# Kernel optimization log

Hardware: AMD Instinct MI355X
Metric: run time of the kernel (lower is better)

The kernel has to match this reference:

```python
import jax, jax.numpy as jnp
import numpy as np

Q = 0.96  # fixed draw from min(1, Uniform(0.9, 1.02)) for determinism


def _tf_quantile(t, q):
    # flatten all but batch dim, linear-interp quantile along last axis
    b = t.shape[0]
    flat = t.reshape(b, -1)
    srt = jnp.sort(flat, axis=-1)
    rank = float(flat.shape[-1])
    pos = (rank - 1.0) * q
    lo = int(np.floor(pos))
    hi = int(np.ceil(pos))
    w_hi = jnp.asarray(pos - lo, dtype=t.dtype)
    return (1.0 - w_hi) * srt[:, lo] + w_hi * srt[:, hi]  # (B,)


def reference(x, v, uu, mask):
    # x: (B, C, L), v: (B, 4, L), uu: (B, Cu, L, L), mask: (B, 1, L) bool
    B, C, L = x.shape
    maskb = mask.astype(bool)
    mask_sum = jnp.sum(maskb.astype(x.dtype), axis=-1)  # (B, 1)
    maxlen = _tf_quantile(mask_sum, Q)                  # (B,) valid count per sample

    # random permutation via argsort: valid slots filled with -1, invalid with U(0,1)
    key = jax.random.key(42)
    rand = jax.random.uniform(key, maskb.shape, dtype=x.dtype)
    rand = jnp.where(~maskb, rand, jnp.asarray(-1.0, x.dtype))
    perm = jnp.argsort(-rand, axis=-1)                  # descending, (B, 1, L)

    mask_p = jnp.take_along_axis(maskb, perm, axis=-1)
    x_p = jnp.take_along_axis(x, jnp.broadcast_to(perm, x.shape), axis=-1)
    v_p = jnp.take_along_axis(v, jnp.broadcast_to(perm, v.shape), axis=-1)
    # permute both particle axes of pairwise features uu: uu[b,c,perm[i],perm[j]]
    uu_p = jnp.take_along_axis(uu, jnp.broadcast_to(perm[:, :, :, None], uu.shape), axis=-2)
    uu_p = jnp.take_along_axis(uu_p, jnp.broadcast_to(perm[:, :, None, :], uu.shape), axis=-1)

    maxlen = jnp.maximum(jnp.round(maxlen), 1.0)        # (B,)
    ml = maxlen.astype(jnp.int32)[:, None, None]        # (B, 1, 1)
    ch = jnp.arange(L, dtype=jnp.int32)[None, None, :]  # (1, 1, L)
    keep = ch < ml                                       # identity when maxlen >= L (tf.cond)
    mask_p = jnp.where(keep, mask_p, jnp.zeros_like(mask_p))
    x_p = jnp.where(keep, x_p, jnp.zeros_like(x_p))
    v_p = jnp.where(keep, v_p, jnp.zeros_like(v_p))
    return (x_p, v_p, mask_p, uu_p)


def setup_inputs() -> dict:
    key = jax.random.key(0)
    k1, k2, k3, k4 = jax.random.split(key, 4)
    B, C, L, Cu = 64, 64, 512, 4
    x = jax.random.normal(k1, (B, C, L), dtype=jnp.float32)
    v = jax.random.normal(k2, (B, 4, L), dtype=jnp.float32)
    uu = jax.random.normal(k3, (B, Cu, L, L), dtype=jnp.float32)
    # realistic ragged mask: first `length` particles valid per sample
    lengths = jax.random.randint(k4, (B, 1, 1), L // 2, L + 1)
    mask = (jnp.arange(L)[None, None, :] < lengths)
    return {"x": x, "v": v, "uu": uu, "mask": mask}
```

## Files before the change

kernel.cpp:

```cpp
#include <hip/hip_runtime.h>
#include <stdint.h>

#define LEN 512
#define NB 64
#define NCX 64
#define NCV 4
#define NCU 4

typedef float f4 __attribute__((ext_vector_type(4)));

__device__ __forceinline__ uint32_t rotl32(uint32_t v, int r) {
  return (v << r) | (v >> (32 - r));
}

__device__ __forceinline__ void threefry2x32_k042(uint32_t c0, uint32_t c1,
                                                  uint32_t& o0, uint32_t& o1) {
  const uint32_t ks0 = 0u, ks1 = 42u;
  const uint32_t ks2 = 0u ^ 42u ^ 0x1BD11BDAu;
  uint32_t x0 = c0 + ks0;
  uint32_t x1 = c1 + ks1;
#define TF_ROUND(R) { x0 += x1; x1 = rotl32(x1, R); x1 ^= x0; }
  TF_ROUND(13) TF_ROUND(15) TF_ROUND(26) TF_ROUND(6)
  x0 += ks1; x1 += ks2 + 1u;
  TF_ROUND(17) TF_ROUND(29) TF_ROUND(16) TF_ROUND(24)
  x0 += ks2; x1 += ks0 + 2u;
  TF_ROUND(13) TF_ROUND(15) TF_ROUND(26) TF_ROUND(6)
  x0 += ks0; x1 += ks1 + 3u;
  TF_ROUND(17) TF_ROUND(29) TF_ROUND(16) TF_ROUND(24)
  x0 += ks1; x1 += ks2 + 4u;
  TF_ROUND(13) TF_ROUND(15) TF_ROUND(26) TF_ROUND(6)
  x0 += ks2; x1 += ks0 + 5u;
#undef TF_ROUND
  o0 = x0; o1 = x1;
}

__global__ __launch_bounds__(LEN) void build_perm(const void* __restrict__ mask,
                                                  int* __restrict__ src,
                                                  int* __restrict__ dst,
                                                  int* __restrict__ ml_arr,
                                                  float* __restrict__ mask_out) {
  const int b = blockIdx.x;
  const int l = threadIdx.x;
  const int wave = l >> 6, lane = l & 63;
  __shared__ alignas(16) uint32_t s_pack[LEN];
  __shared__ int wsum[8];
  __shared__ int woff[9];

  const uint32_t w0 = ((const uint32_t*)mask)[0];
  bool valid;
  if (w0 == 1u) {
    valid = ((const int*)mask)[b * LEN + l] != 0;
  } else if (w0 == 0x3F800000u) {
    valid = ((const float*)mask)[b * LEN + l] != 0.0f;
  } else {
    valid = ((const unsigned char*)mask)[b * LEN + l] != 0;
  }
  const bool inv = !valid;

  uint32_t o0, o1;
  threefry2x32_k042(0u, (uint32_t)(b * LEN + l), o0, o1);
  const uint32_t bits = o0 ^ o1;
  const uint32_t ui = (bits >> 9) | 0x3F800000u;
  const uint32_t me = ((ui & 0x7FFFFFu) << 9) | (uint32_t)(511 - l);

  const unsigned long long bal = __ballot(inv);
  const int lower = __popcll(bal & ((1ull << lane) - 1ull));
  if (lane == 0) wsum[wave] = __popcll(bal);
  __syncthreads();
  if (l == 0) {
    int acc = 0;
    for (int w = 0; w < 8; ++w) { woff[w] = acc; acc += wsum[w]; }
    woff[8] = acc;
  }
  __syncthreads();
  const int n_inv = woff[8];
  const int inv_before = woff[wave] + lower;
  if (inv) {
    s_pack[inv_before] = me;
  }
  __syncthreads();

  int pos;
  if (inv) {
    int rank = 0;
    int j = 0;
    for (; j + 8 <= n_inv; j += 8) {
      const uint4 p0 = *(const uint4*)&s_pack[j];
      const uint4 p1 = *(const uint4*)&s_pack[j + 4];
      rank += (int)(p0.x > me) + (int)(p0.y > me) + (int)(p0.z > me) +
              (int)(p0.w > me) + (int)(p1.x > me) + (int)(p1.y > me) +
              (int)(p1.z > me) + (int)(p1.w > me);
    }
    for (; j < n_inv; ++j) rank += (int)(s_pack[j] > me);
    pos = rank;
  } else {
    pos = n_inv + (l - inv_before);
  }
  src[b * LEN + pos] = l;
  dst[b * LEN + l] = pos;

  const int nv = LEN - n_inv;
  const int ml = nv < 1 ? 1 : nv;
  if (l == 0) ml_arr[b] = ml;
  mask_out[b * LEN + l] = (l >= n_inv && l < ml) ? 1.0f : 0.0f;
}

__global__ __launch_bounds__(256) void uu_perm(const float* __restrict__ in,
                                               float* __restrict__ out,
                                               const float* __restrict__ xin,
                                               const float* __restrict__ vin,
                                               float* __restrict__ xout,
                                               float* __restrict__ vout,
                                               const int* __restrict__ src,
                                               const int* __restrict__ ml_arr) {
  __shared__ float s_row[4][LEN];
  const int tid = threadIdx.x;
  const int wave = tid >> 6, lane = tid & 63;
  const int b = blockIdx.x >> 6;
  const int k = blockIdx.x & 63;
  const int orow0 = blockIdx.x * 32 + wave * 8;
  const int i0 = orow0 & (LEN - 1);
  const long plane = (long)(orow0 & ~(LEN - 1)) * LEN;
  const int* srcb_full = src + b * LEN;

  int rs[8];
#pragma unroll
  for (int r = 0; r < 8; ++r) rs[r] = srcb_full[i0 + r];

  f4 a0[8], a1[8];
#pragma unroll
  for (int r = 0; r < 8; ++r) {
    const float* ip = in + plane + (long)rs[r] * LEN + lane * 4;
    a0[r] = *(const f4*)(ip);
    a1[r] = *(const f4*)(ip + 256);
  }

  int c0[4], c1[4];
#pragma unroll
  for (int kk = 0; kk < 4; ++kk) {
    c0[kk] = srcb_full[lane * 4 + kk];
    c1[kk] = srcb_full[256 + lane * 4 + kk];
  }

  float* myrow = &s_row[wave][0];
  float* op0 = out + plane + (long)i0 * LEN + lane * 4;

#pragma unroll
  for (int r = 0; r < 8; ++r) {
    *(f4*)(myrow + lane * 4) = a0[r];
    *(f4*)(myrow + 256 + lane * 4) = a1[r];
    f4 q0, q1;
    q0.x = myrow[c0[0]]; q0.y = myrow[c0[1]]; q0.z = myrow[c0[2]]; q0.w = myrow[c0[3]];
    q1.x = myrow[c1[0]]; q1.y = myrow[c1[1]]; q1.z = myrow[c1[2]]; q1.w = myrow[c1[3]];
    f4* op = (f4*)(op0 + (long)r * LEN);
    op[0] = q0;
    *(f4*)((float*)op + 256) = q1;
  }

  const int ml = ml_arr[b];
  {
    const float* xrow = xin + (long)((b << 6) + k) * LEN;
    float* orow = xout + (long)((b << 6) + k) * LEN;
    for (int p = tid; p < LEN; p += 256) {
      orow[p] = (p < ml) ? xrow[srcb_full[p]] : 0.0f;
    }
  }
  if (k < NCV) {
    const float* vrow = vin + (long)((b << 2) + k) * LEN;
    float* orow = vout + (long)((b << 2) + k) * LEN;
    for (int p = tid; p < LEN; p += 256) {
      orow[p] = (p < ml) ? vrow[srcb_full[p]] : 0.0f;
    }
  }
}

extern "C" void kernel_launch(void* const* d_in, const int* in_sizes, int n_in,
                              void* d_out, int out_size, void* d_ws, size_t ws_size,
                              hipStream_t stream) {
  const float* x  = (const float*)d_in[0];
  const float* v  = (const float*)d_in[1];
  const float* uu = (const float*)d_in[2];
  const void*  mask = d_in[3];

  float* out   = (float*)d_out;
  float* out_x = out;
  float* out_v = out + 2097152;
  float* out_m = out + 2228224;
  float* out_u = out + 2260992;

  int* src = (int*)d_ws;
  int* dst = src + NB * LEN;
  int* ml  = dst + NB * LEN;

  build_perm<<<NB, LEN, 0, stream>>>(mask, src, dst, ml, out_m);

  uu_perm<<<(NB * NCU * LEN) / 32, 256, 0, stream>>>(
      uu, out_u, x, v, out_x, out_v, src, ml);
}
```

Before: 115.8 us.

## Stream uu rows into triple-buffered LDS via global_load_lds with vmcnt pipelining

```diff
diff --git a/kernel.cpp b/kernel.cpp
--- a/kernel.cpp
+++ b/kernel.cpp
@@ -105,6 +105,12 @@
   mask_out[b * LEN + l] = (l >= n_inv && l < ml) ? 1.0f : 0.0f;
 }
 
+__device__ __forceinline__ void gload16(const float* g, float* l) {
+  __builtin_amdgcn_global_load_lds(
+      (const __attribute__((address_space(1))) void*)g,
+      (__attribute__((address_space(3))) void*)l, 16, 0, 0);
+}
+
 __global__ __launch_bounds__(256) void uu_perm(const float* __restrict__ in,
                                                float* __restrict__ out,
                                                const float* __restrict__ xin,
@@ -113,7 +119,7 @@
                                                float* __restrict__ vout,
                                                const int* __restrict__ src,
                                                const int* __restrict__ ml_arr) {
-  __shared__ float s_row[4][LEN];
+  __shared__ alignas(16) float s_buf[4][3][LEN];
   const int tid = threadIdx.x;
   const int wave = tid >> 6, lane = tid & 63;
   const int b = blockIdx.x >> 6;
@@ -127,14 +133,6 @@
 #pragma unroll
   for (int r = 0; r < 8; ++r) rs[r] = srcb_full[i0 + r];
 
-  f4 a0[8], a1[8];
-#pragma unroll
-  for (int r = 0; r < 8; ++r) {
-    const float* ip = in + plane + (long)rs[r] * LEN + lane * 4;
-    a0[r] = *(const f4*)(ip);
-    a1[r] = *(const f4*)(ip + 256);
-  }
-
   int c0[4], c1[4];
 #pragma unroll
   for (int kk = 0; kk < 4; ++kk) {
@@ -142,20 +140,42 @@
     c1[kk] = srcb_full[256 + lane * 4 + kk];
   }
 
-  float* myrow = &s_row[wave][0];
   float* op0 = out + plane + (long)i0 * LEN + lane * 4;
 
-#pragma unroll
-  for (int r = 0; r < 8; ++r) {
-    *(f4*)(myrow + lane * 4) = a0[r];
-    *(f4*)(myrow + 256 + lane * 4) = a1[r];
-    f4 q0, q1;
-    q0.x = myrow[c0[0]]; q0.y = myrow[c0[1]]; q0.z = myrow[c0[2]]; q0.w = myrow[c0[3]];
-    q1.x = myrow[c1[0]]; q1.y = myrow[c1[1]]; q1.z = myrow[c1[2]]; q1.w = myrow[c1[3]];
-    f4* op = (f4*)(op0 + (long)r * LEN);
-    op[0] = q0;
-    *(f4*)((float*)op + 256) = q1;
-  }
+#define ISSUE(r, s) do {                                              \
+    const float* gp = in + plane + (long)rs[r] * LEN + lane * 4;      \
+    float* lp = &s_buf[wave][s][0];                                   \
+    gload16(gp, lp);                                                  \
+    gload16(gp + 256, lp + 256);                                      \
+  } while (0)
+
+#define WAITV(n) asm volatile("s_waitcnt vmcnt(" #n ")" ::: "memory")
+
+#define GATHER(r, s) do {                                             \
+    const float* myrow = &s_buf[wave][s][0];                          \
+    f4 q0, q1;                                                        \
+    q0.x = myrow[c0[0]]; q0.y = myrow[c0[1]];                         \
+    q0.z = myrow[c0[2]]; q0.w = myrow[c0[3]];                         \
+    q1.x = myrow[c1[0]]; q1.y = myrow[c1[1]];                         \
+    q1.z = myrow[c1[2]]; q1.w = myrow[c1[3]];                         \
+    f4* op = (f4*)(op0 + (long)(r) * LEN);                            \
+    op[0] = q0;                                                       \
+    *(f4*)((float*)op + 256) = q1;                                    \
+  } while (0)
+
+  ISSUE(0, 0);
+  ISSUE(1, 1);
+  ISSUE(2, 2); WAITV(4); GATHER(0, 0);
+  ISSUE(3, 0); WAITV(6); GATHER(1, 1);
+  ISSUE(4, 1); WAITV(8); GATHER(2, 2);
+  ISSUE(5, 2); WAITV(8); GATHER(3, 0);
+  ISSUE(6, 0); WAITV(8); GATHER(4, 1);
+  ISSUE(7, 1); WAITV(8); GATHER(5, 2);
+               WAITV(6); GATHER(6, 0);
+               WAITV(4); GATHER(7, 1);
+#undef ISSUE
+#undef WAITV
+#undef GATHER
 
   const int ml = ml_arr[b];
   {
```

Result: no change. 117.1 us, median of 4 (+1.1%).

## Fuse permutation build into uu gather kernel, recompute perm per block

Applied to the files above, without the earlier changes.

```diff
diff --git a/kernel.cpp b/kernel.cpp
--- a/kernel.cpp
+++ b/kernel.cpp
@@ -34,98 +34,106 @@
   o0 = x0; o1 = x1;
 }
 
-__global__ __launch_bounds__(LEN) void build_perm(const void* __restrict__ mask,
-                                                  int* __restrict__ src,
-                                                  int* __restrict__ dst,
-                                                  int* __restrict__ ml_arr,
-                                                  float* __restrict__ mask_out) {
-  const int b = blockIdx.x;
-  const int l = threadIdx.x;
-  const int wave = l >> 6, lane = l & 63;
+__global__ __launch_bounds__(256) void fused_trim(
+    const float* __restrict__ in, float* __restrict__ out,
+    const float* __restrict__ xin, const float* __restrict__ vin,
+    float* __restrict__ xout, float* __restrict__ vout,
+    float* __restrict__ mask_out, const void* __restrict__ mask) {
   __shared__ alignas(16) uint32_t s_pack[LEN];
+  __shared__ int s_src[LEN];
+  __shared__ float s_row[4][LEN];
   __shared__ int wsum[8];
   __shared__ int woff[9];
 
+  const int tid = threadIdx.x;
+  const int wave = tid >> 6, lane = tid & 63;
+  const int blk = blockIdx.x;
+  const int b = blk >> 6;
+  const int k = blk & 63;
+
+  const int l0 = tid, l1 = tid + 256;
   const uint32_t w0 = ((const uint32_t*)mask)[0];
-  bool valid;
+  bool valid0, valid1;
   if (w0 == 1u) {
-    valid = ((const int*)mask)[b * LEN + l] != 0;
+    valid0 = ((const int*)mask)[b * LEN + l0] != 0;
+    valid1 = ((const int*)mask)[b * LEN + l1] != 0;
   } else if (w0 == 0x3F800000u) {
-    valid = ((const float*)mask)[b * LEN + l] != 0.0f;
+    valid0 = ((const float*)mask)[b * LEN + l0] != 0.0f;
+    valid1 = ((const float*)mask)[b * LEN + l1] != 0.0f;
   } else {
-    valid = ((const unsigned char*)mask)[b * LEN + l] != 0;
-  }
-  const bool inv = !valid;
-
-  uint32_t o0, o1;
-  threefry2x32_k042(0u, (uint32_t)(b * LEN + l), o0, o1);
-  const uint32_t bits = o0 ^ o1;
-  const uint32_t ui = (bits >> 9) | 0x3F800000u;
-  const uint32_t me = ((ui & 0x7FFFFFu) << 9) | (uint32_t)(511 - l);
-
-  const unsigned long long bal = __ballot(inv);
-  const int lower = __popcll(bal & ((1ull << lane) - 1ull));
-  if (lane == 0) wsum[wave] = __popcll(bal);
-  __syncthreads();
-  if (l == 0) {
+    valid0 = ((const unsigned char*)mask)[b * LEN + l0] != 0;
+    valid1 = ((const unsigned char*)mask)[b * LEN + l1] != 0;
+  }
+  const bool inv0 = !valid0, inv1 = !valid1;
+
+  uint32_t a, c, me0, me1;
+  threefry2x32_k042(0u, (uint32_t)(b * LEN + l0), a, c);
+  me0 = ((((a ^ c) >> 9) & 0x7FFFFFu) << 9) | (uint32_t)(511 - l0);
+  threefry2x32_k042(0u, (uint32_t)(b * LEN + l1), a, c);
+  me1 = ((((a ^ c) >> 9) & 0x7FFFFFu) << 9) | (uint32_t)(511 - l1);
+
+  const unsigned long long bal0 = __ballot(inv0);
+  const unsigned long long bal1 = __ballot(inv1);
+  const unsigned long long lmask = (1ull << lane) - 1ull;
+  const int lower0 = __popcll(bal0 & lmask);
+  const int lower1 = __popcll(bal1 & lmask);
+  if (lane == 0) {
+    wsum[wave] = __popcll(bal0);
+    wsum[4 + wave] = __popcll(bal1);
+  }
+  __syncthreads();
+  if (tid == 0) {
     int acc = 0;
     for (int w = 0; w < 8; ++w) { woff[w] = acc; acc += wsum[w]; }
     woff[8] = acc;
   }
   __syncthreads();
   const int n_inv = woff[8];
-  const int inv_before = woff[wave] + lower;
-  if (inv) {
-    s_pack[inv_before] = me;
-  }
-  __syncthreads();
-
-  int pos;
-  if (inv) {
-    int rank = 0;
+  const int ib0 = woff[wave] + lower0;
+  const int ib1 = woff[4 + wave] + lower1;
+  if (inv0) s_pack[ib0] = me0;
+  if (inv1) s_pack[ib1] = me1;
+  __syncthreads();
+
+  int r0 = 0, r1 = 0;
+  if (inv0 || inv1) {
     int j = 0;
     for (; j + 8 <= n_inv; j += 8) {
       const uint4 p0 = *(const uint4*)&s_pack[j];
       const uint4 p1 = *(const uint4*)&s_pack[j + 4];
-      rank += (int)(p0.x > me) + (int)(p0.y > me) + (int)(p0.z > me) +
-              (int)(p0.w > me) + (int)(p1.x > me) + (int)(p1.y > me) +
-              (int)(p1.z > me) + (int)(p1.w > me);
-    }
-    for (; j < n_inv; ++j) rank += (int)(s_pack[j] > me);
-    pos = rank;
-  } else {
-    pos = n_inv + (l - inv_before);
-  }
-  src[b * LEN + pos] = l;
-  dst[b * LEN + l] = pos;
+      r0 += (int)(p0.x > me0) + (int)(p0.y > me0) + (int)(p0.z > me0) +
+            (int)(p0.w > me0) + (int)(p1.x > me0) + (int)(p1.y > me0) +
+            (int)(p1.z > me0) + (int)(p1.w > me0);
+      r1 += (int)(p0.x > me1) + (int)(p0.y > me1) + (int)(p0.z > me1) +
+            (int)(p0.w > me1) + (int)(p1.x > me1) + (int)(p1.y > me1) +
+            (int)(p1.z > me1) + (int)(p1.w > me1);
+    }
+    for (; j < n_inv; ++j) {
+      const uint32_t kj = s_pack[j];
+      r0 += (int)(kj > me0);
+      r1 += (int)(kj > me1);
+    }
+  }
+  const int pos0 = inv0 ? r0 : n_inv + (l0 - ib0);
+  const int pos1 = inv1 ? r1 : n_inv + (l1 - ib1);
+  s_src[pos0] = l0;
+  s_src[pos1] = l1;
 
   const int nv = LEN - n_inv;
   const int ml = nv < 1 ? 1 : nv;
-  if (l == 0) ml_arr[b] = ml;
-  mask_out[b * LEN + l] = (l >= n_inv && l < ml) ? 1.0f : 0.0f;
-}
-
-__global__ __launch_bounds__(256) void uu_perm(const float* __restrict__ in,
-                                               float* __restrict__ out,
-                                               const float* __restrict__ xin,
-                                               const float* __restrict__ vin,
-                                               float* __restrict__ xout,
-                                               float* __restrict__ vout,
-                                               const int* __restrict__ src,
-                                               const int* __restrict__ ml_arr) {
-  __shared__ float s_row[4][LEN];
-  const int tid = threadIdx.x;
-  const int wave = tid >> 6, lane = tid & 63;
-  const int b = blockIdx.x >> 6;
-  const int k = blockIdx.x & 63;
-  const int orow0 = blockIdx.x * 32 + wave * 8;
+  if (k == 0) {
+    mask_out[b * LEN + l0] = (l0 >= n_inv && l0 < ml) ? 1.0f : 0.0f;
+    mask_out[b * LEN + l1] = (l1 >= n_inv && l1 < ml) ? 1.0f : 0.0f;
+  }
+  __syncthreads();
+
+  const int orow0 = blk * 32 + wave * 8;
   const int i0 = orow0 & (LEN - 1);
   const long plane = (long)(orow0 & ~(LEN - 1)) * LEN;
-  const int* srcb_full = src + b * LEN;
 
   int rs[8];
 #pragma unroll
-  for (int r = 0; r < 8; ++r) rs[r] = srcb_full[i0 + r];
+  for (int r = 0; r < 8; ++r) rs[r] = s_src[i0 + r];
 
   f4 a0[8], a1[8];
 #pragma unroll
@@ -138,8 +146,8 @@
   int c0[4], c1[4];
 #pragma unroll
   for (int kk = 0; kk < 4; ++kk) {
-    c0[kk] = srcb_full[lane * 4 + kk];
-    c1[kk] = srcb_full[256 + lane * 4 + kk];
+    c0[kk] = s_src[lane * 4 + kk];
+    c1[kk] = s_src[256 + lane * 4 + kk];
   }
 
   float* myrow = &s_row[wave][0];
@@ -157,19 +165,18 @@
     *(f4*)((float*)op + 256) = q1;
   }
 
-  const int ml = ml_arr[b];
   {
     const float* xrow = xin + (long)((b << 6) + k) * LEN;
     float* orow = xout + (long)((b << 6) + k) * LEN;
     for (int p = tid; p < LEN; p += 256) {
-      orow[p] = (p < ml) ? xrow[srcb_full[p]] : 0.0f;
+      orow[p] = (p < ml) ? xrow[s_src[p]] : 0.0f;
     }
   }
   if (k < NCV) {
     const float* vrow = vin + (long)((b << 2) + k) * LEN;
     float* orow = vout + (long)((b << 2) + k) * LEN;
     for (int p = tid; p < LEN; p += 256) {
-      orow[p] = (p < ml) ? vrow[srcb_full[p]] : 0.0f;
+      orow[p] = (p < ml) ? vrow[s_src[p]] : 0.0f;
     }
   }
 }
@@ -188,12 +195,6 @@
   float* out_m = out + 2228224;
   float* out_u = out + 2260992;
 
-  int* src = (int*)d_ws;
-  int* dst = src + NB * LEN;
-  int* ml  = dst + NB * LEN;
-
-  build_perm<<<NB, LEN, 0, stream>>>(mask, src, dst, ml, out_m);
-
-  uu_perm<<<(NB * NCU * LEN) / 32, 256, 0, stream>>>(
-      uu, out_u, x, v, out_x, out_v, src, ml);
-}
+  fused_trim<<<NB * NCU * LEN / 32, 256, 0, stream>>>(
+      uu, out_u, x, v, out_x, out_v, out_m, mask);
+}
```

After: 110.7 us. -4.4%, faster.
